# Performance work log

Hardware: AMD Instinct MI355X
Metric: run time of the kernel (lower is better)

The kernel has to match this reference:

```python
import jax, jax.numpy as jnp
import numpy as np

B, G, K, N = 8, 2048, 32, 6
C = 64  # lc_x feature dim (mapping_size), must be even
SCALE = 10.0
EPS = 1e-8


def setup_inputs() -> dict:
    key = jax.random.key(0)
    k1, k2, k3 = jax.random.split(key, 3)
    lc_x = jax.random.normal(k1, (B, G, C), dtype=jnp.float32)
    knn_x = jax.random.normal(k2, (B, G, K, N), dtype=jnp.float32)
    fourier_B = jax.random.normal(k3, (7, C // 2), dtype=jnp.float32) * SCALE
    return {"lc_x": lc_x, "knn_x": knn_x, "fourier_B": fourier_B}


def reference(lc_x, knn_x, fourier_B):
    # lc_x: [B,G,C], knn_x: [B,G,K,N], fourier_B: [7, C//2]
    lc_normal = lc_x[:, :, 3:6][:, :, None, :]            # [B,G,1,3], broadcasts over K
    lc_line = lc_x / jnp.linalg.norm(lc_x, axis=2, keepdims=True)
    lc_line = jnp.transpose(lc_line, (0, 2, 1))            # [B,C,G]

    knn_product = knn_x[..., 3:6]                          # [B,G,K,3]
    lcn_b = jnp.broadcast_to(lc_normal, knn_product.shape)
    knn_cross = jnp.cross(knn_product, lcn_b, axis=-1)     # [B,G,K,3]
    knn_dot = jnp.sum(knn_product * lc_normal, axis=-1, keepdims=True)  # [B,G,K,1]
    knn_line = jnp.concatenate([knn_product, knn_cross, knn_dot], axis=-1)  # [B,G,K,7]

    # Fourier feature mapping (4D path: permute to channels-last already holds)
    x_proj = knn_line @ fourier_B                          # [B,G,K,C/2]
    ff = jnp.concatenate([jnp.sin(2 * jnp.pi * x_proj), jnp.cos(2 * jnp.pi * x_proj)], axis=-1)
    ff = jnp.sign(ff) * jnp.abs(ff) ** 5                   # [B,G,K,C]
    knn_f = jnp.transpose(ff, (0, 3, 1, 2))                # [B,C,G,K]

    # K_ANP over last dim (K); torch.std is unbiased (ddof=1); .item() -> stop_gradient
    std = jnp.std(knn_f, axis=-1, keepdims=True, ddof=1)
    p = 2.0 + jax.lax.stop_gradient(jnp.log1p(jnp.mean(std)))
    norm = jnp.sum(jnp.abs(knn_f) ** p, axis=-1, keepdims=True) ** (1.0 / p)  # [B,C,G,1]
    lc = norm / (norm + EPS)  # sum over size-1 last dim equals norm itself
    e_x = jnp.exp(lc)                                      # [B,C,G,1]
    up = jnp.mean(knn_f * e_x, axis=-1)                    # [B,C,G]
    down = jnp.mean(e_x, axis=-1)                          # [B,C,G]
    anp = up / down

    kl = anp + jnp.mean(knn_f, axis=-1)                    # [B,C,G] (squeeze is no-op: B,C,G>1)
    kl = kl / jnp.linalg.norm(kl, axis=-1, keepdims=True)  # normalize over G
    line_element = kl - lc_line
    return jnp.concatenate([line_element, lc_line], axis=1)  # [B,2C,G]
```

## Files before the change

### kernel.cpp

```cpp
#include <hip/hip_runtime.h>
#include <hip/hip_bf16.h>


#if __has_builtin(__builtin_amdgcn_fractf)
  #define FRACT(x) __builtin_amdgcn_fractf(x)
#else
  #define FRACT(x) ((x) - floorf(x))
#endif

__global__ __launch_bounds__(256, 8) void line_pass1(
    const float* __restrict__ lc_x,
    const float* __restrict__ knn_x,
    const float* __restrict__ fB,
    float* __restrict__ out)
{
    const int wave = threadIdx.x >> 6;
    const int lane = threadIdx.x & 63;
    const int half = lane >> 5;
    const int jj   = lane & 31;
    const int sbid = (blockIdx.x & 7) * 512 + (blockIdx.x >> 3);
    const int bg   = sbid * 4 + wave;
    const int b    = bg >> 11;
    const int g    = bg & 2047;

    const float fb0 = fB[0*32 + jj];
    const float fb1 = fB[1*32 + jj];
    const float fb2 = fB[2*32 + jj];
    const float fb3 = fB[3*32 + jj];
    const float fb4 = fB[4*32 + jj];
    const float fb5 = fB[5*32 + jj];
    const float fb6 = fB[6*32 + jj];

    const float* lcr = lc_x + (size_t)bg * 64;
    const float lc = lcr[lane];
    float ssum = lc * lc;
    #pragma unroll
    for (int off = 32; off; off >>= 1) ssum += __shfl_xor(ssum, off, 64);
    const float lcline = lc / sqrtf(ssum);

    const float n0 = lcr[3];
    const float n1 = lcr[4];
    const float n2 = lcr[5];

    const float e0 = fmaf(fb6, n0, fmaf(fb5,  n1, fmaf(fb4, -n2, fb0)));
    const float e1 = fmaf(fb6, n1, fmaf(fb5, -n0, fmaf(fb3,  n2, fb1)));
    const float e2 = fmaf(fb6, n2, fmaf(fb4,  n0, fmaf(fb3, -n1, fb2)));

    __shared__ __align__(16) float4 lv[4][32];
    if (half == 0) {
        const float* kp = knn_x + (size_t)bg * 192 + jj * 6;
        lv[wave][jj] = make_float4(kp[3], kp[4], kp[5], 0.0f);
    }
    asm volatile("s_waitcnt lgkmcnt(0)" ::: "memory");

    float accS[2] = {0.0f, 0.0f};
    float accC[2] = {0.0f, 0.0f};
    const float4* myk = &lv[wave][half];
    #pragma unroll
    for (int i = 0; i < 16; ++i) {
        const float4 p = myk[2 * i];
        const float x = fmaf(e2, p.z, fmaf(e1, p.y, e0 * p.x));

        const float ts = FRACT(x);
        const float tc = FRACT(x + 0.25f);
        const float s  = __builtin_amdgcn_sinf(ts);
        const float cc = __builtin_amdgcn_sinf(tc);
        const float s2 = s * s,  s4 = s2 * s2;
        const float q2 = cc * cc, q4 = q2 * q2;
        accS[i & 1] = fmaf(s4, s,  accS[i & 1]);
        accC[i & 1] = fmaf(q4, cc, accC[i & 1]);
    }

    const float aS = accS[0] + accS[1];
    const float aC = accC[0] + accC[1];
    const float totS = aS + __shfl_xor(aS, 32, 64);
    const float totC = aC + __shfl_xor(aC, 32, 64);
    const float klraw = (half ? totC : totS) * 0.0625f;

    const size_t obase = ((size_t)b * 128) * 2048 + g;
    out[obase + (size_t)lane * 2048]        = klraw;
    out[obase + (size_t)(64 + lane) * 2048] = lcline;
}

__global__ __launch_bounds__(256) void line_pass2(float* __restrict__ out)
{
    const int b = blockIdx.x >> 6;
    const int c = blockIdx.x & 63;
    float*       kl = out + ((size_t)b * 128 + c) * 2048;
    const float* ll = out + ((size_t)b * 128 + 64 + c) * 2048;

    float v[8];
    float ss = 0.0f;
    #pragma unroll
    for (int i = 0; i < 8; ++i) {
        v[i] = kl[threadIdx.x + i * 256];
        ss = fmaf(v[i], v[i], ss);
    }
    #pragma unroll
    for (int off = 32; off; off >>= 1) ss += __shfl_xor(ss, off, 64);

    __shared__ float wsum[4];
    if ((threadIdx.x & 63) == 0) wsum[threadIdx.x >> 6] = ss;
    __syncthreads();
    const float tot = wsum[0] + wsum[1] + wsum[2] + wsum[3];
    const float rn  = 1.0f / sqrtf(tot);

    #pragma unroll
    for (int i = 0; i < 8; ++i) {
        const int idx = threadIdx.x + i * 256;
        kl[idx] = fmaf(v[i], rn, -ll[idx]);
    }
}

extern "C" void kernel_launch(void* const* d_in, const int* in_sizes, int n_in,
                              void* d_out, int out_size, void* d_ws, size_t ws_size,
                              hipStream_t stream) {
    const float* lc_x  = (const float*)d_in[0];
    const float* knn_x = (const float*)d_in[1];
    const float* fB    = (const float*)d_in[2];
    float* out = (float*)d_out;

    line_pass1<<<4096, 256, 0, stream>>>(lc_x, knn_x, fB, out);
    line_pass2<<<512, 256, 0, stream>>>(out);
}
```

Baseline: 23.81 us.

## Process 16 points per block and stage outputs in LDS for coalesced stores

Each block now handles 16 (b,g) points instead of 4, with each wave looping over 4 points. Results go to a shared transpose buffer so the output, stored as [B,128,G], can be written with contiguous float4 stores along G instead of strided scalar stores. The second pass is also vectorised to float4 loads and stores. In exchange, each wave does more serial work, LDS use rises, and a block-wide barrier is added.

```diff
diff --git a/kernel.cpp b/kernel.cpp
--- a/kernel.cpp
+++ b/kernel.cpp
@@ -18,10 +18,13 @@
     const int lane = threadIdx.x & 63;
     const int half = lane >> 5;
     const int jj   = lane & 31;
-    const int sbid = (blockIdx.x & 7) * 512 + (blockIdx.x >> 3);
-    const int bg   = sbid * 4 + wave;
-    const int b    = bg >> 11;
-    const int g    = bg & 2047;
+    const int sbid = (blockIdx.x & 7) * 128 + (blockIdx.x >> 3);
+    const int bg0  = sbid * 16;
+    const int b    = bg0 >> 11;
+    const int g0   = bg0 & 2047;
+
+    __shared__ __align__(16) float4 lv[4][4][32];
+    __shared__ float klbuf[128][17];
 
     const float fb0 = fB[0*32 + jj];
     const float fb1 = fB[1*32 + jj];
@@ -31,85 +34,102 @@
     const float fb5 = fB[5*32 + jj];
     const float fb6 = fB[6*32 + jj];
 
-    const float* lcr = lc_x + (size_t)bg * 64;
-    const float lc = lcr[lane];
-    float ssum = lc * lc;
+    float lcv[4], pp0[4], pp1[4], pp2[4];
     #pragma unroll
-    for (int off = 32; off; off >>= 1) ssum += __shfl_xor(ssum, off, 64);
-    const float lcline = lc / sqrtf(ssum);
-
-    const float n0 = lcr[3];
-    const float n1 = lcr[4];
-    const float n2 = lcr[5];
-
-    const float e0 = fmaf(fb6, n0, fmaf(fb5,  n1, fmaf(fb4, -n2, fb0)));
-    const float e1 = fmaf(fb6, n1, fmaf(fb5, -n0, fmaf(fb3,  n2, fb1)));
-    const float e2 = fmaf(fb6, n2, fmaf(fb4,  n0, fmaf(fb3, -n1, fb2)));
-
-    __shared__ __align__(16) float4 lv[4][32];
-    if (half == 0) {
-        const float* kp = knn_x + (size_t)bg * 192 + jj * 6;
-        lv[wave][jj] = make_float4(kp[3], kp[4], kp[5], 0.0f);
+    for (int i = 0; i < 4; ++i) {
+        const int bg = bg0 + wave * 4 + i;
+        lcv[i] = lc_x[(size_t)bg * 64 + lane];
+        if (half == 0) {
+            const float* kp = knn_x + (size_t)bg * 192 + jj * 6;
+            pp0[i] = kp[3]; pp1[i] = kp[4]; pp2[i] = kp[5];
+        }
+    }
+    #pragma unroll
+    for (int i = 0; i < 4; ++i) {
+        if (half == 0)
+            lv[wave][i][jj] = make_float4(pp0[i], pp1[i], pp2[i], 0.0f);
     }
     asm volatile("s_waitcnt lgkmcnt(0)" ::: "memory");
 
-    float accS[2] = {0.0f, 0.0f};
-    float accC[2] = {0.0f, 0.0f};
-    const float4* myk = &lv[wave][half];
     #pragma unroll
-    for (int i = 0; i < 16; ++i) {
-        const float4 p = myk[2 * i];
-        const float x = fmaf(e2, p.z, fmaf(e1, p.y, e0 * p.x));
+    for (int i = 0; i < 4; ++i) {
+        const int bg  = bg0 + wave * 4 + i;
+        const int col = wave * 4 + i;
+        const float* lcr = lc_x + (size_t)bg * 64;
+        const float n0 = lcr[3];
+        const float n1 = lcr[4];
+        const float n2 = lcr[5];
 
-        const float ts = FRACT(x);
-        const float tc = FRACT(x + 0.25f);
-        const float s  = __builtin_amdgcn_sinf(ts);
-        const float cc = __builtin_amdgcn_sinf(tc);
-        const float s2 = s * s,  s4 = s2 * s2;
-        const float q2 = cc * cc, q4 = q2 * q2;
-        accS[i & 1] = fmaf(s4, s,  accS[i & 1]);
-        accC[i & 1] = fmaf(q4, cc, accC[i & 1]);
+        float ssum = lcv[i] * lcv[i];
+        #pragma unroll
+        for (int off = 32; off; off >>= 1) ssum += __shfl_xor(ssum, off, 64);
+        klbuf[64 + lane][col] = lcv[i] / sqrtf(ssum);
+
+        const float e0 = fmaf(fb6, n0, fmaf(fb5,  n1, fmaf(fb4, -n2, fb0)));
+        const float e1 = fmaf(fb6, n1, fmaf(fb5, -n0, fmaf(fb3,  n2, fb1)));
+        const float e2 = fmaf(fb6, n2, fmaf(fb4,  n0, fmaf(fb3, -n1, fb2)));
+
+        float accS0 = 0.f, accS1 = 0.f, accC0 = 0.f, accC1 = 0.f;
+        const float4* myk = &lv[wave][i][half];
+        #pragma unroll
+        for (int t = 0; t < 16; ++t) {
+            const float4 p = myk[2 * t];
+            const float x = fmaf(e2, p.z, fmaf(e1, p.y, e0 * p.x));
+            const float ts = FRACT(x);
+            const float tc = FRACT(x + 0.25f);
+            const float s  = __builtin_amdgcn_sinf(ts);
+            const float cq = __builtin_amdgcn_sinf(tc);
+            const float s2 = s * s,   s4 = s2 * s2;
+            const float q2 = cq * cq, q4 = q2 * q2;
+            if (t & 1) { accS1 = fmaf(s4, s, accS1); accC1 = fmaf(q4, cq, accC1); }
+            else       { accS0 = fmaf(s4, s, accS0); accC0 = fmaf(q4, cq, accC0); }
+        }
+        const float aS = accS0 + accS1;
+        const float aC = accC0 + accC1;
+        const float totS = aS + __shfl_xor(aS, 32, 64);
+        const float totC = aC + __shfl_xor(aC, 32, 64);
+        klbuf[lane][col] = (half ? totC : totS) * 0.0625f;
     }
 
-    const float aS = accS[0] + accS[1];
-    const float aC = accC[0] + accC[1];
-    const float totS = aS + __shfl_xor(aS, 32, 64);
-    const float totC = aC + __shfl_xor(aC, 32, 64);
-    const float klraw = (half ? totC : totS) * 0.0625f;
+    __syncthreads();
 
-    const size_t obase = ((size_t)b * 128) * 2048 + g;
-    out[obase + (size_t)lane * 2048]        = klraw;
-    out[obase + (size_t)(64 + lane) * 2048] = lcline;
+    const int c  = threadIdx.x >> 1;
+    const int j0 = (threadIdx.x & 1) * 8;
+    float o[8];
+    #pragma unroll
+    for (int q = 0; q < 8; ++q) o[q] = klbuf[c][j0 + q];
+    float* dst = out + ((size_t)b * 128 + c) * 2048 + g0 + j0;
+    *(float4*)(dst + 0) = make_float4(o[0], o[1], o[2], o[3]);
+    *(float4*)(dst + 4) = make_float4(o[4], o[5], o[6], o[7]);
 }
 
 __global__ __launch_bounds__(256) void line_pass2(float* __restrict__ out)
 {
     const int b = blockIdx.x >> 6;
     const int c = blockIdx.x & 63;
-    float*       kl = out + ((size_t)b * 128 + c) * 2048;
-    const float* ll = out + ((size_t)b * 128 + 64 + c) * 2048;
+    float4*       kl = (float4*)(out + ((size_t)b * 128 + c) * 2048);
+    const float4* ll = (const float4*)(out + ((size_t)b * 128 + 64 + c) * 2048);
+    const int t = threadIdx.x;
 
-    float v[8];
-    float ss = 0.0f;
-    #pragma unroll
-    for (int i = 0; i < 8; ++i) {
-        v[i] = kl[threadIdx.x + i * 256];
-        ss = fmaf(v[i], v[i], ss);
-    }
+    const float4 v0 = kl[t];
+    const float4 v1 = kl[t + 256];
+    float ss = v0.x*v0.x + v0.y*v0.y + v0.z*v0.z + v0.w*v0.w
+             + v1.x*v1.x + v1.y*v1.y + v1.z*v1.z + v1.w*v1.w;
     #pragma unroll
     for (int off = 32; off; off >>= 1) ss += __shfl_xor(ss, off, 64);
 
     __shared__ float wsum[4];
-    if ((threadIdx.x & 63) == 0) wsum[threadIdx.x >> 6] = ss;
+    if ((t & 63) == 0) wsum[t >> 6] = ss;
     __syncthreads();
     const float tot = wsum[0] + wsum[1] + wsum[2] + wsum[3];
     const float rn  = 1.0f / sqrtf(tot);
 
-    #pragma unroll
-    for (int i = 0; i < 8; ++i) {
-        const int idx = threadIdx.x + i * 256;
-        kl[idx] = fmaf(v[i], rn, -ll[idx]);
-    }
+    const float4 l0 = ll[t];
+    const float4 l1 = ll[t + 256];
+    kl[t]       = make_float4(fmaf(v0.x, rn, -l0.x), fmaf(v0.y, rn, -l0.y),
+                              fmaf(v0.z, rn, -l0.z), fmaf(v0.w, rn, -l0.w));
+    kl[t + 256] = make_float4(fmaf(v1.x, rn, -l1.x), fmaf(v1.y, rn, -l1.y),
+                              fmaf(v1.z, rn, -l1.z), fmaf(v1.w, rn, -l1.w));
 }
 
 extern "C" void kernel_launch(void* const* d_in, const int* in_sizes, int n_in,
@@ -120,6 +140,6 @@
     const float* fB    = (const float*)d_in[2];
     float* out = (float*)d_out;
 
-    line_pass1<<<4096, 256, 0, stream>>>(lc_x, knn_x, fB, out);
+    line_pass1<<<1024, 256, 0, stream>>>(lc_x, knn_x, fB, out);
     line_pass2<<<512, 256, 0, stream>>>(out);
 }
```

After: 24.21 us. Within noise of the previous version (+1.7%).
